# Performance work log

Hardware: AMD Instinct MI355X
Metric: run time of the kernel (lower is better)

The kernel has to match this reference:

```python
import jax, jax.numpy as jnp
import numpy as np

B, SQ, SKV, D, H = 4, 1024, 2048, 1024, 16
HD = D // H


def setup_inputs() -> dict:
    key = jax.random.key(0)
    ks = jax.random.split(key, 8)
    std = 0.02
    return {
        "hidden_states": jax.random.normal(ks[0], (B, SQ, D), jnp.float32),
        "encoder_hidden_states": jax.random.normal(ks[1], (B, SKV, D), jnp.float32),
        "attention_mask_kv": jnp.zeros((B, 1, 1, SKV), jnp.float32),
        "q_attn_w": jax.random.normal(ks[2], (D, D), jnp.float32) * std,
        "q_attn_b": jnp.zeros((D,), jnp.float32),
        "c_attn_w": jax.random.normal(ks[3], (D, 2 * D), jnp.float32) * std,
        "c_attn_b": jnp.zeros((2 * D,), jnp.float32),
        "c_proj_w": jax.random.normal(ks[4], (D, D), jnp.float32) * std,
        "c_proj_b": jnp.zeros((D,), jnp.float32),
    }


def _split_heads(x):
    # [B, S, D] -> [B, H, S, HD]
    b, s, _ = x.shape
    return x.reshape(b, s, H, HD).transpose(0, 2, 1, 3)


def reference(hidden_states, encoder_hidden_states, attention_mask_kv,
              q_attn_w, q_attn_b, c_attn_w, c_attn_b, c_proj_w, c_proj_b):
    # Conv1D is x @ W + b (weights stored transposed vs nn.Linear)
    query = hidden_states @ q_attn_w + q_attn_b                     # [B,SQ,D]
    kv = encoder_hidden_states @ c_attn_w + c_attn_b                # [B,SKV,2D]
    key, value = kv[..., :D], kv[..., D:]

    q = _split_heads(query)   # [B,H,SQ,HD]
    k = _split_heads(key)     # [B,H,SKV,HD]
    v = _split_heads(value)   # [B,H,SKV,HD]

    # scale by sqrt(head_dim) == value.size(-1)**0.5 in original
    attn_weights = jnp.einsum('bhqd,bhkd->bhqk', q, k) / jnp.sqrt(jnp.float32(HD))
    attn_weights = attn_weights + attention_mask_kv
    attn_weights = jax.nn.softmax(attn_weights, axis=-1)            # [B,H,SQ,SKV]
    # dropout in eval mode = identity
    attn_output = jnp.einsum('bhqk,bhkd->bhqd', attn_weights, v)    # [B,H,SQ,HD]
    attn_output = attn_output.transpose(0, 2, 1, 3).reshape(B, SQ, D)
    attn_output = attn_output @ c_proj_w + c_proj_b
    return attn_output, attn_weights
```

## Files before the change

### kernel.cpp

```cpp
#include <hip/hip_runtime.h>
#include <stdint.h>

#define B_ 4
#define SQ_ 1024
#define SKV_ 2048
#define D_ 1024
#define H_ 16
#define HD_ 64

typedef short v8s __attribute__((ext_vector_type(8)));
typedef float v4f __attribute__((ext_vector_type(4)));

__device__ __forceinline__ unsigned short f2bf(float f) {
  union { float f; unsigned int u; } c; c.f = f;
  unsigned int u = c.u;
  return (unsigned short)((u + 0x7fffu + ((u >> 16) & 1u)) >> 16);
}

__device__ __forceinline__ void gll16(const void* g, void* l) {
  __builtin_amdgcn_global_load_lds((__attribute__((address_space(1))) void*)g,
                                   (__attribute__((address_space(3))) void*)l,
                                   16, 0, 0);
}

__global__ void f2bf_k(const float* __restrict__ in, unsigned short* __restrict__ out, int n4) {
  int i = blockIdx.x * 256 + threadIdx.x;
  if (i < n4) {
    const float4 v = ((const float4*)in)[i];
    ushort4 o;
    o.x = f2bf(v.x); o.y = f2bf(v.y); o.z = f2bf(v.z); o.w = f2bf(v.w);
    ((ushort4*)out)[i] = o;
  }
}

__global__ void tconv_k(const float* __restrict__ W, unsigned short* __restrict__ Wt, int K, int N) {
  __shared__ float t[32][33];
  const int n0 = blockIdx.x * 32, k0 = blockIdx.y * 32;
  const int tx = threadIdx.x, ty = threadIdx.y;
#pragma unroll
  for (int r = 0; r < 32; r += 8)
    t[ty + r][tx] = W[(size_t)(k0 + ty + r) * N + (n0 + tx)];
  __syncthreads();
#pragma unroll
  for (int r = 0; r < 32; r += 8)
    Wt[(size_t)(n0 + ty + r) * K + (k0 + tx)] = f2bf(t[tx][ty + r]);
}

template <int EPI>
__global__ void gemm_bt(const unsigned short* __restrict__ A,
                        const unsigned short* __restrict__ Bt,
                        const float* __restrict__ bias,
                        unsigned short* __restrict__ O0,
                        unsigned short* __restrict__ O1,
                        float* __restrict__ OF,
                        int M, int N, int K) {
  __shared__ __align__(16) unsigned short As[128 * 32];
  __shared__ __align__(16) unsigned short Bs[128 * 32];
  const int tid = threadIdx.x;
  const int lane = tid & 63;
  const int w = tid >> 6;
  const int wm = w >> 1, wn = w & 1;
  const int l15 = lane & 15, l4 = lane >> 4;
  const int m0 = blockIdx.x * 128;
  const int n0 = blockIdx.y * 128;

  v4f acc[4][4];
#pragma unroll
  for (int i = 0; i < 4; i++)
#pragma unroll
    for (int j = 0; j < 4; j++) acc[i][j] = (v4f){0.f, 0.f, 0.f, 0.f};

  const int sr = tid >> 2;
  const int sc = (tid & 3) * 8;
  const unsigned short* gA = A + (size_t)(m0 + sr) * K + sc;
  const unsigned short* gB = Bt + (size_t)(n0 + sr) * K + sc;
  unsigned short* lA = &As[tid * 8];
  unsigned short* lB = &Bs[tid * 8];

  for (int k0 = 0; k0 < K; k0 += 32) {
    __syncthreads();
    gll16(gA + k0, lA);
    gll16(gA + (size_t)64 * K + k0, lA + 64 * 32);
    gll16(gB + k0, lB);
    gll16(gB + (size_t)64 * K + k0, lB + 64 * 32);
    __syncthreads();
    v8s af[4], bf[4];
#pragma unroll
    for (int mi = 0; mi < 4; mi++)
      af[mi] = *(const v8s*)&As[(wm * 64 + mi * 16 + l15) * 32 + l4 * 8];
#pragma unroll
    for (int ni = 0; ni < 4; ni++)
      bf[ni] = *(const v8s*)&Bs[(wn * 64 + ni * 16 + l15) * 32 + l4 * 8];
#pragma unroll
    for (int mi = 0; mi < 4; mi++)
#pragma unroll
      for (int ni = 0; ni < 4; ni++)
        acc[mi][ni] = __builtin_amdgcn_mfma_f32_16x16x32_bf16(af[mi], bf[ni], acc[mi][ni], 0, 0, 0);
  }

#pragma unroll
  for (int mi = 0; mi < 4; mi++) {
#pragma unroll
    for (int ni = 0; ni < 4; ni++) {
#pragma unroll
      for (int j = 0; j < 4; j++) {
        const int m = m0 + wm * 64 + mi * 16 + l4 * 4 + j;
        const int n = n0 + wn * 64 + ni * 16 + l15;
        const float v = acc[mi][ni][j] + bias[n];
        if (EPI == 0) {
          const int b = m >> 10, sq = m & 1023, h = n >> 6, hd = n & 63;
          O0[(((size_t)(b * H_ + h)) * SQ_ + sq) * HD_ + hd] = f2bf(v);
        } else if (EPI == 1) {
          const int b = m >> 11, skv = m & 2047;
          if (n < D_) {
            const int h = n >> 6, hd = n & 63;
            O0[(((size_t)(b * H_ + h)) * SKV_ + skv) * HD_ + hd] = f2bf(v);
          } else {
            const int n2 = n - D_;
            const int h = n2 >> 6, hd = n2 & 63;
            O1[(((size_t)(b * H_ + h)) * HD_ + hd) * SKV_ + skv] = f2bf(v);
          }
        } else {
          OF[(size_t)m * N + n] = v;
        }
      }
    }
  }
}

__global__ __launch_bounds__(256)
void attn_k(const unsigned short* __restrict__ Qb,
            const unsigned short* __restrict__ Kb,
            const unsigned short* __restrict__ Vtb,
            const float* __restrict__ mask,
            float* __restrict__ AW,
            unsigned short* __restrict__ X) {
  __shared__ __align__(16) unsigned short Ks[64 * 64];
  __shared__ __align__(16) unsigned short Vs[64 * 64];
  __shared__ __align__(16) unsigned short Ps[4][16 * 64];
  __shared__ __align__(16) float mk[SKV_];

  const int tid = threadIdx.x;
  const int lane = tid & 63;
  const int w = tid >> 6;
  const int l15 = lane & 15, l4 = lane >> 4;
  const int qt = blockIdx.x, h = blockIdx.y, b = blockIdx.z;
  const int bh = b * H_ + h;

  for (int i = tid; i < SKV_ / 4; i += 256)
    ((float4*)mk)[i] = ((const float4*)(mask + (size_t)b * SKV_))[i];

  const int qrow = qt * 64 + w * 16 + l15;
  const size_t qbase = ((size_t)bh * SQ_ + qrow) * HD_;
  const v8s qf0 = *(const v8s*)&Qb[qbase + l4 * 8];
  const v8s qf1 = *(const v8s*)&Qb[qbase + 32 + l4 * 8];

  const int srow = tid >> 3;
  const int sg = tid & 7;
  const size_t kgbase = (size_t)bh * SKV_ * HD_;
  const size_t vgbase = (size_t)bh * HD_ * SKV_;

  float ml[4], ll[4];
#pragma unroll
  for (int j = 0; j < 4; j++) { ml[j] = -1e30f; ll[j] = 0.f; }

  for (int t = 0; t < SKV_ / 64; ++t) {
    const int kv0 = t * 64;
    __syncthreads();
    gll16(&Kb[kgbase + (size_t)(kv0 + srow) * HD_ + (sg ^ (srow & 7)) * 8], &Ks[tid * 8]);
    gll16(&Kb[kgbase + (size_t)(kv0 + srow + 32) * HD_ + (sg ^ ((srow + 32) & 7)) * 8], &Ks[2048 + tid * 8]);
    __syncthreads();

    v4f s[4];
#pragma unroll
    for (int kf = 0; kf < 4; kf++) {
      const int kr = kf * 16 + l15;
      const v8s b0 = *(const v8s*)&Ks[kr * 64 + ((l4 ^ (kr & 7)) * 8)];
      const v8s b1 = *(const v8s*)&Ks[kr * 64 + (((l4 + 4) ^ (kr & 7)) * 8)];
      v4f a = (v4f){0.f, 0.f, 0.f, 0.f};
      a = __builtin_amdgcn_mfma_f32_16x16x32_bf16(qf0, b0, a, 0, 0, 0);
      a = __builtin_amdgcn_mfma_f32_16x16x32_bf16(qf1, b1, a, 0, 0, 0);
      s[kf] = a;
    }
    float sv[4][4];
#pragma unroll
    for (int kf = 0; kf < 4; kf++) {
      const float mval = mk[kv0 + kf * 16 + l15];
#pragma unroll
      for (int j = 0; j < 4; j++) sv[kf][j] = s[kf][j] * 0.125f + mval;
    }
#pragma unroll
    for (int j = 0; j < 4; j++) {
      const float mx = fmaxf(fmaxf(sv[0][j], sv[1][j]), fmaxf(sv[2][j], sv[3][j]));
      const float mn = fmaxf(ml[j], mx);
      ll[j] = ll[j] * __expf(ml[j] - mn)
            + __expf(sv[0][j] - mn) + __expf(sv[1][j] - mn)
            + __expf(sv[2][j] - mn) + __expf(sv[3][j] - mn);
      ml[j] = mn;
    }
  }
#pragma unroll
  for (int j = 0; j < 4; j++) {
    float m = ml[j], l = ll[j];
#pragma unroll
    for (int off = 1; off < 16; off <<= 1) {
      const float mo = __shfl_xor(m, off);
      const float lo = __shfl_xor(l, off);
      const float mn = fmaxf(m, mo);
      l = l * __expf(m - mn) + lo * __expf(mo - mn);
      m = mn;
    }
    ml[j] = m;
    ll[j] = 1.f / l;
  }

  v4f oa[4];
#pragma unroll
  for (int nf = 0; nf < 4; nf++) oa[nf] = (v4f){0.f, 0.f, 0.f, 0.f};

  float* awbase = AW + ((size_t)bh * SQ_ + qt * 64 + w * 16) * SKV_;

  for (int t = 0; t < SKV_ / 64; ++t) {
    const int kv0 = t * 64;
    __syncthreads();
    gll16(&Kb[kgbase + (size_t)(kv0 + srow) * HD_ + (sg ^ (srow & 7)) * 8], &Ks[tid * 8]);
    gll16(&Kb[kgbase + (size_t)(kv0 + srow + 32) * HD_ + (sg ^ ((srow + 32) & 7)) * 8], &Ks[2048 + tid * 8]);
    gll16(&Vtb[vgbase + (size_t)srow * SKV_ + kv0 + (sg ^ (srow & 7)) * 8], &Vs[tid * 8]);
    gll16(&Vtb[vgbase + (size_t)(srow + 32) * SKV_ + kv0 + (sg ^ ((srow + 32) & 7)) * 8], &Vs[2048 + tid * 8]);
    __syncthreads();

    v4f s[4];
#pragma unroll
    for (int kf = 0; kf < 4; kf++) {
      const int kr = kf * 16 + l15;
      const v8s b0 = *(const v8s*)&Ks[kr * 64 + ((l4 ^ (kr & 7)) * 8)];
      const v8s b1 = *(const v8s*)&Ks[kr * 64 + (((l4 + 4) ^ (kr & 7)) * 8)];
      v4f a = (v4f){0.f, 0.f, 0.f, 0.f};
      a = __builtin_amdgcn_mfma_f32_16x16x32_bf16(qf0, b0, a, 0, 0, 0);
      a = __builtin_amdgcn_mfma_f32_16x16x32_bf16(qf1, b1, a, 0, 0, 0);
      s[kf] = a;
    }
#pragma unroll
    for (int kf = 0; kf < 4; kf++) {
      const int kvc = kf * 16 + l15;
      const float mval = mk[kv0 + kvc];
#pragma unroll
      for (int j = 0; j < 4; j++) {
        const float svv = s[kf][j] * 0.125f + mval;
        const float p = __expf(svv - ml[j]) * ll[j];
        const int q = l4 * 4 + j;
        awbase[(size_t)q * SKV_ + kv0 + kvc] = p;
        Ps[w][q * 64 + (((kvc >> 3) ^ (q & 7)) * 8) + (kvc & 7)] = f2bf(p);
      }
    }
    asm volatile("s_waitcnt lgkmcnt(0)" ::: "memory");
    __builtin_amdgcn_sched_barrier(0);
#pragma unroll
    for (int kk = 0; kk < 2; kk++) {
      const v8s pf = *(const v8s*)&Ps[w][l15 * 64 + (((l4 + kk * 4) ^ (l15 & 7)) * 8)];
#pragma unroll
      for (int nf = 0; nf < 4; nf++) {
        const int hd = nf * 16 + l15;
        const v8s vf = *(const v8s*)&Vs[hd * 64 + (((l4 + kk * 4) ^ (hd & 7)) * 8)];
        oa[nf] = __builtin_amdgcn_mfma_f32_16x16x32_bf16(pf, vf, oa[nf], 0, 0, 0);
      }
    }
  }

#pragma unroll
  for (int nf = 0; nf < 4; nf++) {
#pragma unroll
    for (int j = 0; j < 4; j++) {
      const int q = qt * 64 + w * 16 + l4 * 4 + j;
      X[((size_t)b * SQ_ + q) * D_ + h * HD_ + nf * 16 + l15] = f2bf(oa[nf][j]);
    }
  }
}

extern "C" void kernel_launch(void* const* d_in, const int* in_sizes, int n_in,
                              void* d_out, int out_size, void* d_ws, size_t ws_size,
                              hipStream_t stream) {
  (void)in_sizes; (void)n_in; (void)out_size; (void)ws_size;
  const float* hidden = (const float*)d_in[0];
  const float* enc    = (const float*)d_in[1];
  const float* mask   = (const float*)d_in[2];
  const float* qw     = (const float*)d_in[3];
  const float* qb     = (const float*)d_in[4];
  const float* cw     = (const float*)d_in[5];
  const float* cb     = (const float*)d_in[6];
  const float* pw     = (const float*)d_in[7];
  const float* pb     = (const float*)d_in[8];

  float* out = (float*)d_out;
  float* aw  = out + (size_t)B_ * SQ_ * D_;

  char* ws = (char*)d_ws;
  unsigned short* hbf = (unsigned short*)(ws + (size_t)(0u)  * (1u << 20));
  unsigned short* ebf = (unsigned short*)(ws + (size_t)(8u)  * (1u << 20));
  unsigned short* qwt = (unsigned short*)(ws + (size_t)(24u) * (1u << 20));
  unsigned short* cat = (unsigned short*)(ws + (size_t)(26u) * (1u << 20));
  unsigned short* cpt = (unsigned short*)(ws + (size_t)(30u) * (1u << 20));
  unsigned short* Qb  = (unsigned short*)(ws + (size_t)(32u) * (1u << 20));
  unsigned short* Kb  = (unsigned short*)(ws + (size_t)(40u) * (1u << 20));
  unsigned short* Vtb = (unsigned short*)(ws + (size_t)(56u) * (1u << 20));
  unsigned short* Xb  = (unsigned short*)(ws + (size_t)(72u) * (1u << 20));

  hipLaunchKernelGGL(f2bf_k, dim3((B_ * SQ_ * D_ / 4 + 255) / 256), dim3(256), 0, stream,
                     hidden, hbf, B_ * SQ_ * D_ / 4);
  hipLaunchKernelGGL(f2bf_k, dim3((B_ * SKV_ * D_ / 4 + 255) / 256), dim3(256), 0, stream,
                     enc, ebf, B_ * SKV_ * D_ / 4);
  hipLaunchKernelGGL(tconv_k, dim3(D_ / 32, D_ / 32), dim3(32, 8), 0, stream, qw, qwt, D_, D_);
  hipLaunchKernelGGL(tconv_k, dim3(2 * D_ / 32, D_ / 32), dim3(32, 8), 0, stream, cw, cat, D_, 2 * D_);
  hipLaunchKernelGGL(tconv_k, dim3(D_ / 32, D_ / 32), dim3(32, 8), 0, stream, pw, cpt, D_, D_);

  hipLaunchKernelGGL(gemm_bt<0>, dim3(B_ * SQ_ / 128, D_ / 128), dim3(256), 0, stream,
                     hbf, qwt, qb, Qb, (unsigned short*)nullptr, (float*)nullptr, B_ * SQ_, D_, D_);
  hipLaunchKernelGGL(gemm_bt<1>, dim3(B_ * SKV_ / 128, 2 * D_ / 128), dim3(256), 0, stream,
                     ebf, cat, cb, Kb, Vtb, (float*)nullptr, B_ * SKV_, 2 * D_, D_);
  hipLaunchKernelGGL(attn_k, dim3(SQ_ / 64, H_, B_), dim3(256), 0, stream,
                     Qb, Kb, Vtb, mask, aw, Xb);
  hipLaunchKernelGGL(gemm_bt<2>, dim3(B_ * SQ_ / 128, D_ / 128), dim3(256), 0, stream,
                     Xb, cpt, pb, (unsigned short*)nullptr, (unsigned short*)nullptr, out, B_ * SQ_, D_, D_);
}
```

Baseline: 824.1 us.

## Rework GEMM tiling/epilogue and attention to direct global loads with transposed MFMA

The GEMM now loads a BK=64 tile with an XOR swizzle, and its epilogue stages results through LDS so stores are vectorized (the V-transpose path writes ushort4 directly). The attention kernel drops the LDS staging of K, V and the mask. K/V fragments come straight from global memory, and the operands of QK^T are swapped so each lane holds 4 consecutive kv columns. This allows float4 attention-weight stores, exp2-based softmax with a log-sum-exp constant, and a block-id remap to group heads for L2 reuse. The goal is to cut the uncoalesced scalar stores of the large fp32 attention-weight output and remove block syncs. The cost is redundant per-wave global/L2 reads of K and V.

```diff
diff --git a/kernel.cpp b/kernel.cpp
--- a/kernel.cpp
+++ b/kernel.cpp
@@ -11,17 +11,20 @@
 typedef short v8s __attribute__((ext_vector_type(8)));
 typedef float v4f __attribute__((ext_vector_type(4)));
 
-__device__ __forceinline__ unsigned short f2bf(float f) {
+static __device__ __forceinline__ unsigned short f2bf(float f) {
   union { float f; unsigned int u; } c; c.f = f;
   unsigned int u = c.u;
   return (unsigned short)((u + 0x7fffu + ((u >> 16) & 1u)) >> 16);
 }
 
-__device__ __forceinline__ void gll16(const void* g, void* l) {
+static __device__ __forceinline__ void gll16(const void* g, void* l) {
   __builtin_amdgcn_global_load_lds((__attribute__((address_space(1))) void*)g,
                                    (__attribute__((address_space(3))) void*)l,
                                    16, 0, 0);
 }
+
+#define LGKM0() do { asm volatile("s_waitcnt lgkmcnt(0)" ::: "memory"); \
+                     __builtin_amdgcn_sched_barrier(0); } while (0)
 
 __global__ void f2bf_k(const float* __restrict__ in, unsigned short* __restrict__ out, int n4) {
   int i = blockIdx.x * 256 + threadIdx.x;
@@ -47,15 +50,18 @@
 }
 
 template <int EPI>
-__global__ void gemm_bt(const unsigned short* __restrict__ A,
-                        const unsigned short* __restrict__ Bt,
-                        const float* __restrict__ bias,
-                        unsigned short* __restrict__ O0,
-                        unsigned short* __restrict__ O1,
-                        float* __restrict__ OF,
-                        int M, int N, int K) {
-  __shared__ __align__(16) unsigned short As[128 * 32];
-  __shared__ __align__(16) unsigned short Bs[128 * 32];
+__global__ __launch_bounds__(256)
+void gemm_bt(const unsigned short* __restrict__ A,
+             const unsigned short* __restrict__ Bt,
+             const float* __restrict__ bias,
+             unsigned short* __restrict__ O0,
+             unsigned short* __restrict__ O1,
+             float* __restrict__ OF,
+             int M, int N, int K) {
+  __shared__ __align__(16) char smem[32768];
+  unsigned short* As = (unsigned short*)smem;
+  unsigned short* Bs = (unsigned short*)(smem + 16384);
+
   const int tid = threadIdx.x;
   const int lane = tid & 63;
   const int w = tid >> 6;
@@ -70,59 +76,106 @@
 #pragma unroll
     for (int j = 0; j < 4; j++) acc[i][j] = (v4f){0.f, 0.f, 0.f, 0.f};
 
-  const int sr = tid >> 2;
-  const int sc = (tid & 3) * 8;
-  const unsigned short* gA = A + (size_t)(m0 + sr) * K + sc;
-  const unsigned short* gB = Bt + (size_t)(n0 + sr) * K + sc;
-  unsigned short* lA = &As[tid * 8];
-  unsigned short* lB = &Bs[tid * 8];
-
-  for (int k0 = 0; k0 < K; k0 += 32) {
+  const int sr = tid >> 3;
+  const int sg = tid & 7;
+  const int scol = (sg ^ (sr & 7)) * 8;
+  const unsigned short* gA = A + (size_t)(m0 + sr) * K + scol;
+  const unsigned short* gB = Bt + (size_t)(n0 + sr) * K + scol;
+  char* lA = (char*)As + tid * 16;
+  char* lB = (char*)Bs + tid * 16;
+
+  for (int k0 = 0; k0 < K; k0 += 64) {
     __syncthreads();
-    gll16(gA + k0, lA);
-    gll16(gA + (size_t)64 * K + k0, lA + 64 * 32);
-    gll16(gB + k0, lB);
-    gll16(gB + (size_t)64 * K + k0, lB + 64 * 32);
+#pragma unroll
+    for (int r = 0; r < 4; r++) {
+      gll16(gA + (size_t)(r * 32) * K + k0, lA + r * 4096);
+      gll16(gB + (size_t)(r * 32) * K + k0, lB + r * 4096);
+    }
     __syncthreads();
-    v8s af[4], bf[4];
-#pragma unroll
-    for (int mi = 0; mi < 4; mi++)
-      af[mi] = *(const v8s*)&As[(wm * 64 + mi * 16 + l15) * 32 + l4 * 8];
+#pragma unroll
+    for (int kk = 0; kk < 2; kk++) {
+      v8s af[4], bg[4];
+#pragma unroll
+      for (int mi = 0; mi < 4; mi++) {
+        const int row = wm * 64 + mi * 16 + l15;
+        af[mi] = *(const v8s*)((const char*)As + row * 128 + (((kk * 4 + l4) ^ (row & 7)) * 16));
+      }
+#pragma unroll
+      for (int ni = 0; ni < 4; ni++) {
+        const int row = wn * 64 + ni * 16 + l15;
+        bg[ni] = *(const v8s*)((const char*)Bs + row * 128 + (((kk * 4 + l4) ^ (row & 7)) * 16));
+      }
+#pragma unroll
+      for (int mi = 0; mi < 4; mi++)
+#pragma unroll
+        for (int ni = 0; ni < 4; ni++)
+          acc[mi][ni] = __builtin_amdgcn_mfma_f32_16x16x32_bf16(af[mi], bg[ni], acc[mi][ni], 0, 0, 0);
+    }
+  }
+
+  __syncthreads();
+
+  float bsel[4];
+#pragma unroll
+  for (int ni = 0; ni < 4; ni++) bsel[ni] = bias[n0 + wn * 64 + ni * 16 + l15];
+
+  if (EPI == 1 && n0 >= D_) {
+#pragma unroll
+    for (int mi = 0; mi < 4; mi++) {
+#pragma unroll
+      for (int ni = 0; ni < 4; ni++) {
+        const int n2 = n0 + wn * 64 + ni * 16 + l15 - D_;
+        const int hh = n2 >> 6, hd = n2 & 63;
+        const int m = m0 + wm * 64 + mi * 16 + l4 * 4;
+        const int bb = m >> 11, skv = m & 2047;
+        ushort4 o;
+        o.x = f2bf(acc[mi][ni][0] + bsel[ni]);
+        o.y = f2bf(acc[mi][ni][1] + bsel[ni]);
+        o.z = f2bf(acc[mi][ni][2] + bsel[ni]);
+        o.w = f2bf(acc[mi][ni][3] + bsel[ni]);
+        *(ushort4*)&O1[(((size_t)(bb * H_ + hh)) * HD_ + hd) * SKV_ + skv] = o;
+      }
+    }
+    return;
+  }
+
+  float* T = (float*)(smem + w * 4352);
+#pragma unroll
+  for (int mi = 0; mi < 4; mi++) {
+    LGKM0();
 #pragma unroll
     for (int ni = 0; ni < 4; ni++)
-      bf[ni] = *(const v8s*)&Bs[(wn * 64 + ni * 16 + l15) * 32 + l4 * 8];
-#pragma unroll
-    for (int mi = 0; mi < 4; mi++)
-#pragma unroll
-      for (int ni = 0; ni < 4; ni++)
-        acc[mi][ni] = __builtin_amdgcn_mfma_f32_16x16x32_bf16(af[mi], bf[ni], acc[mi][ni], 0, 0, 0);
-  }
-
-#pragma unroll
-  for (int mi = 0; mi < 4; mi++) {
-#pragma unroll
-    for (int ni = 0; ni < 4; ni++) {
-#pragma unroll
-      for (int j = 0; j < 4; j++) {
-        const int m = m0 + wm * 64 + mi * 16 + l4 * 4 + j;
-        const int n = n0 + wn * 64 + ni * 16 + l15;
-        const float v = acc[mi][ni][j] + bias[n];
+#pragma unroll
+      for (int j = 0; j < 4; j++)
+        T[(l4 * 4 + j) * 68 + ni * 16 + l15] = acc[mi][ni][j] + bsel[ni];
+    LGKM0();
+    const int m = m0 + wm * 64 + mi * 16 + l15;
+    if (EPI == 2) {
+#pragma unroll
+      for (int s = 0; s < 4; s++) {
+        const int c = l4 * 4 + s * 16;
+        *(float4*)&OF[(size_t)m * N + n0 + wn * 64 + c] = *(const float4*)&T[l15 * 68 + c];
+      }
+    } else {
+      const int hh = (n0 + wn * 64) >> 6;
+#pragma unroll
+      for (int s = 0; s < 2; s++) {
+        const int c = l4 * 8 + s * 32;
+        const float4 u = *(const float4*)&T[l15 * 68 + c];
+        const float4 v = *(const float4*)&T[l15 * 68 + c + 4];
+        ushort4 o0, o1;
+        o0.x = f2bf(u.x); o0.y = f2bf(u.y); o0.z = f2bf(u.z); o0.w = f2bf(u.w);
+        o1.x = f2bf(v.x); o1.y = f2bf(v.y); o1.z = f2bf(v.z); o1.w = f2bf(v.w);
+        size_t base;
         if (EPI == 0) {
-          const int b = m >> 10, sq = m & 1023, h = n >> 6, hd = n & 63;
-          O0[(((size_t)(b * H_ + h)) * SQ_ + sq) * HD_ + hd] = f2bf(v);
-        } else if (EPI == 1) {
-          const int b = m >> 11, skv = m & 2047;
-          if (n < D_) {
-            const int h = n >> 6, hd = n & 63;
-            O0[(((size_t)(b * H_ + h)) * SKV_ + skv) * HD_ + hd] = f2bf(v);
-          } else {
-            const int n2 = n - D_;
-            const int h = n2 >> 6, hd = n2 & 63;
-            O1[(((size_t)(b * H_ + h)) * HD_ + hd) * SKV_ + skv] = f2bf(v);
-          }
+          const int bb = m >> 10, sq = m & 1023;
+          base = (((size_t)(bb * H_ + hh)) * SQ_ + sq) * HD_ + c;
         } else {
-          OF[(size_t)m * N + n] = v;
+          const int bb = m >> 11, skv = m & 2047;
+          base = (((size_t)(bb * H_ + hh)) * SKV_ + skv) * HD_ + c;
         }
+        ushort4* dst = (ushort4*)&O0[base];
+        dst[0] = o0; dst[1] = o1;
       }
     }
   }
@@ -135,133 +188,111 @@
             const float* __restrict__ mask,
             float* __restrict__ AW,
             unsigned short* __restrict__ X) {
-  __shared__ __align__(16) unsigned short Ks[64 * 64];
-  __shared__ __align__(16) unsigned short Vs[64 * 64];
   __shared__ __align__(16) unsigned short Ps[4][16 * 64];
-  __shared__ __align__(16) float mk[SKV_];
 
   const int tid = threadIdx.x;
   const int lane = tid & 63;
   const int w = tid >> 6;
   const int l15 = lane & 15, l4 = lane >> 4;
-  const int qt = blockIdx.x, h = blockIdx.y, b = blockIdx.z;
+
+  int id = blockIdx.x + 16 * blockIdx.y + 256 * blockIdx.z;
+  id = (id & 7) * 128 + (id >> 3);
+  const int qt = id & 15, h = (id >> 4) & 15, b = id >> 8;
   const int bh = b * H_ + h;
 
-  for (int i = tid; i < SKV_ / 4; i += 256)
-    ((float4*)mk)[i] = ((const float4*)(mask + (size_t)b * SKV_))[i];
-
-  const int qrow = qt * 64 + w * 16 + l15;
-  const size_t qbase = ((size_t)bh * SQ_ + qrow) * HD_;
+  const int q = qt * 64 + w * 16 + l15;
+  const size_t qbase = ((size_t)bh * SQ_ + q) * HD_;
   const v8s qf0 = *(const v8s*)&Qb[qbase + l4 * 8];
   const v8s qf1 = *(const v8s*)&Qb[qbase + 32 + l4 * 8];
 
-  const int srow = tid >> 3;
-  const int sg = tid & 7;
   const size_t kgbase = (size_t)bh * SKV_ * HD_;
   const size_t vgbase = (size_t)bh * HD_ * SKV_;
-
-  float ml[4], ll[4];
-#pragma unroll
-  for (int j = 0; j < 4; j++) { ml[j] = -1e30f; ll[j] = 0.f; }
+  const float* mkb = mask + (size_t)b * SKV_;
+
+  const float c1 = 0.18033688011112042f;
+  const float c2 = 1.4426950408889634f;
+
+  float m2 = -1e30f, l2 = 0.f;
 
   for (int t = 0; t < SKV_ / 64; ++t) {
     const int kv0 = t * 64;
-    __syncthreads();
-    gll16(&Kb[kgbase + (size_t)(kv0 + srow) * HD_ + (sg ^ (srow & 7)) * 8], &Ks[tid * 8]);
-    gll16(&Kb[kgbase + (size_t)(kv0 + srow + 32) * HD_ + (sg ^ ((srow + 32) & 7)) * 8], &Ks[2048 + tid * 8]);
-    __syncthreads();
-
-    v4f s[4];
+    float sv[4][4];
 #pragma unroll
     for (int kf = 0; kf < 4; kf++) {
-      const int kr = kf * 16 + l15;
-      const v8s b0 = *(const v8s*)&Ks[kr * 64 + ((l4 ^ (kr & 7)) * 8)];
-      const v8s b1 = *(const v8s*)&Ks[kr * 64 + (((l4 + 4) ^ (kr & 7)) * 8)];
+      const int kr = kv0 + kf * 16 + l15;
+      const v8s a0 = *(const v8s*)&Kb[kgbase + (size_t)kr * HD_ + l4 * 8];
+      const v8s a1 = *(const v8s*)&Kb[kgbase + (size_t)kr * HD_ + 32 + l4 * 8];
       v4f a = (v4f){0.f, 0.f, 0.f, 0.f};
-      a = __builtin_amdgcn_mfma_f32_16x16x32_bf16(qf0, b0, a, 0, 0, 0);
-      a = __builtin_amdgcn_mfma_f32_16x16x32_bf16(qf1, b1, a, 0, 0, 0);
-      s[kf] = a;
-    }
-    float sv[4][4];
-#pragma unroll
-    for (int kf = 0; kf < 4; kf++) {
-      const float mval = mk[kv0 + kf * 16 + l15];
-#pragma unroll
-      for (int j = 0; j < 4; j++) sv[kf][j] = s[kf][j] * 0.125f + mval;
-    }
-#pragma unroll
-    for (int j = 0; j < 4; j++) {
-      const float mx = fmaxf(fmaxf(sv[0][j], sv[1][j]), fmaxf(sv[2][j], sv[3][j]));
-      const float mn = fmaxf(ml[j], mx);
-      ll[j] = ll[j] * __expf(ml[j] - mn)
-            + __expf(sv[0][j] - mn) + __expf(sv[1][j] - mn)
-            + __expf(sv[2][j] - mn) + __expf(sv[3][j] - mn);
-      ml[j] = mn;
-    }
-  }
-#pragma unroll
-  for (int j = 0; j < 4; j++) {
-    float m = ml[j], l = ll[j];
-#pragma unroll
-    for (int off = 1; off < 16; off <<= 1) {
-      const float mo = __shfl_xor(m, off);
-      const float lo = __shfl_xor(l, off);
-      const float mn = fmaxf(m, mo);
-      l = l * __expf(m - mn) + lo * __expf(mo - mn);
-      m = mn;
-    }
-    ml[j] = m;
-    ll[j] = 1.f / l;
-  }
+      a = __builtin_amdgcn_mfma_f32_16x16x32_bf16(a0, qf0, a, 0, 0, 0);
+      a = __builtin_amdgcn_mfma_f32_16x16x32_bf16(a1, qf1, a, 0, 0, 0);
+      const float4 mk4 = *(const float4*)&mkb[kv0 + kf * 16 + l4 * 4];
+      sv[kf][0] = fmaf(a[0], c1, mk4.x * c2);
+      sv[kf][1] = fmaf(a[1], c1, mk4.y * c2);
+      sv[kf][2] = fmaf(a[2], c1, mk4.z * c2);
+      sv[kf][3] = fmaf(a[3], c1, mk4.w * c2);
+    }
+    float mx = sv[0][0];
+#pragma unroll
+    for (int kf = 0; kf < 4; kf++)
+#pragma unroll
+      for (int j = 0; j < 4; j++) mx = fmaxf(mx, sv[kf][j]);
+    const float mn = fmaxf(m2, mx);
+    float add = 0.f;
+#pragma unroll
+    for (int kf = 0; kf < 4; kf++)
+#pragma unroll
+      for (int j = 0; j < 4; j++) add += exp2f(sv[kf][j] - mn);
+    l2 = l2 * exp2f(m2 - mn) + add;
+    m2 = mn;
+  }
+#pragma unroll
+  for (int off = 16; off < 64; off <<= 1) {
+    const float mo = __shfl_xor(m2, off);
+    const float lo = __shfl_xor(l2, off);
+    const float mn = fmaxf(m2, mo);
+    l2 = l2 * exp2f(m2 - mn) + lo * exp2f(mo - mn);
+    m2 = mn;
+  }
+  const float C = m2 + __log2f(l2);
 
   v4f oa[4];
 #pragma unroll
   for (int nf = 0; nf < 4; nf++) oa[nf] = (v4f){0.f, 0.f, 0.f, 0.f};
 
-  float* awbase = AW + ((size_t)bh * SQ_ + qt * 64 + w * 16) * SKV_;
+  float* awrow = AW + ((size_t)bh * SQ_ + q) * SKV_;
+  unsigned short* PsW = &Ps[w][0];
 
   for (int t = 0; t < SKV_ / 64; ++t) {
     const int kv0 = t * 64;
-    __syncthreads();
-    gll16(&Kb[kgbase + (size_t)(kv0 + srow) * HD_ + (sg ^ (srow & 7)) * 8], &Ks[tid * 8]);
-    gll16(&Kb[kgbase + (size_t)(kv0 + srow + 32) * HD_ + (sg ^ ((srow + 32) & 7)) * 8], &Ks[2048 + tid * 8]);
-    gll16(&Vtb[vgbase + (size_t)srow * SKV_ + kv0 + (sg ^ (srow & 7)) * 8], &Vs[tid * 8]);
-    gll16(&Vtb[vgbase + (size_t)(srow + 32) * SKV_ + kv0 + (sg ^ ((srow + 32) & 7)) * 8], &Vs[2048 + tid * 8]);
-    __syncthreads();
-
-    v4f s[4];
 #pragma unroll
     for (int kf = 0; kf < 4; kf++) {
-      const int kr = kf * 16 + l15;
-      const v8s b0 = *(const v8s*)&Ks[kr * 64 + ((l4 ^ (kr & 7)) * 8)];
-      const v8s b1 = *(const v8s*)&Ks[kr * 64 + (((l4 + 4) ^ (kr & 7)) * 8)];
+      const int kr = kv0 + kf * 16 + l15;
+      const v8s a0 = *(const v8s*)&Kb[kgbase + (size_t)kr * HD_ + l4 * 8];
+      const v8s a1 = *(const v8s*)&Kb[kgbase + (size_t)kr * HD_ + 32 + l4 * 8];
       v4f a = (v4f){0.f, 0.f, 0.f, 0.f};
-      a = __builtin_amdgcn_mfma_f32_16x16x32_bf16(qf0, b0, a, 0, 0, 0);
-      a = __builtin_amdgcn_mfma_f32_16x16x32_bf16(qf1, b1, a, 0, 0, 0);
-      s[kf] = a;
-    }
-#pragma unroll
-    for (int kf = 0; kf < 4; kf++) {
-      const int kvc = kf * 16 + l15;
-      const float mval = mk[kv0 + kvc];
-#pragma unroll
-      for (int j = 0; j < 4; j++) {
-        const float svv = s[kf][j] * 0.125f + mval;
-        const float p = __expf(svv - ml[j]) * ll[j];
-        const int q = l4 * 4 + j;
-        awbase[(size_t)q * SKV_ + kv0 + kvc] = p;
-        Ps[w][q * 64 + (((kvc >> 3) ^ (q & 7)) * 8) + (kvc & 7)] = f2bf(p);
-      }
-    }
-    asm volatile("s_waitcnt lgkmcnt(0)" ::: "memory");
-    __builtin_amdgcn_sched_barrier(0);
+      a = __builtin_amdgcn_mfma_f32_16x16x32_bf16(a0, qf0, a, 0, 0, 0);
+      a = __builtin_amdgcn_mfma_f32_16x16x32_bf16(a1, qf1, a, 0, 0, 0);
+      const float4 mk4 = *(const float4*)&mkb[kv0 + kf * 16 + l4 * 4];
+      float4 p;
+      p.x = exp2f(fmaf(a[0], c1, fmaf(mk4.x, c2, -C)));
+      p.y = exp2f(fmaf(a[1], c1, fmaf(mk4.y, c2, -C)));
+      p.z = exp2f(fmaf(a[2], c1, fmaf(mk4.z, c2, -C)));
+      p.w = exp2f(fmaf(a[3], c1, fmaf(mk4.w, c2, -C)));
+      *(float4*)&awrow[kv0 + kf * 16 + l4 * 4] = p;
+      ushort4 pb;
+      pb.x = f2bf(p.x); pb.y = f2bf(p.y); pb.z = f2bf(p.z); pb.w = f2bf(p.w);
+      const int gby = kf * 32 + l4 * 8;
+      *(ushort4*)((char*)PsW + l15 * 128 + (((gby >> 4) ^ (l15 & 7)) * 16) + (gby & 15)) = pb;
+    }
+    LGKM0();
 #pragma unroll
     for (int kk = 0; kk < 2; kk++) {
-      const v8s pf = *(const v8s*)&Ps[w][l15 * 64 + (((l4 + kk * 4) ^ (l15 & 7)) * 8)];
+      const int c = l4 + 4 * kk;
+      const v8s pf = *(const v8s*)((const char*)PsW + l15 * 128 + ((c ^ (l15 & 7)) * 16));
 #pragma unroll
       for (int nf = 0; nf < 4; nf++) {
         const int hd = nf * 16 + l15;
-        const v8s vf = *(const v8s*)&Vs[hd * 64 + (((l4 + kk * 4) ^ (hd & 7)) * 8)];
+        const v8s vf = *(const v8s*)&Vtb[vgbase + (size_t)hd * SKV_ + kv0 + kk * 32 + l4 * 8];
         oa[nf] = __builtin_amdgcn_mfma_f32_16x16x32_bf16(pf, vf, oa[nf], 0, 0, 0);
       }
     }
@@ -271,9 +302,18 @@
   for (int nf = 0; nf < 4; nf++) {
 #pragma unroll
     for (int j = 0; j < 4; j++) {
-      const int q = qt * 64 + w * 16 + l4 * 4 + j;
-      X[((size_t)b * SQ_ + q) * D_ + h * HD_ + nf * 16 + l15] = f2bf(oa[nf][j]);
-    }
+      const int row = l4 * 4 + j;
+      const int gby = (nf * 16 + l15) * 2;
+      *(unsigned short*)((char*)PsW + row * 128 + (((gby >> 4) ^ (row & 7)) * 16) + (gby & 15)) =
+          f2bf(oa[nf][j]);
+    }
+  }
+  LGKM0();
+#pragma unroll
+  for (int s = 0; s < 2; s++) {
+    const int c = l4 + 4 * s;
+    const v8s xv = *(const v8s*)((const char*)PsW + l15 * 128 + ((c ^ (l15 & 7)) * 16));
+    *(v8s*)&X[((size_t)b * SQ_ + q) * D_ + h * HD_ + c * 8] = xv;
   }
 }
 
```

Result: slower. 1.043 ms (+26.6%).
